# Optimization experiments

Hardware: AMD Instinct MI355X
Metric: run time of the kernel (lower is better)

The kernel has to match this reference:

```python
import jax, jax.numpy as jnp
import numpy as np

B, S, D_MODEL, N_HEADS = 4, 2048, 2048, 16
HEAD_DIM = D_MODEL // N_HEADS  # 128
ROT_HALF = HEAD_DIM // 2       # 64


def _make_rope(max_pos, half_dim, base=10000.0):
    inv_freq = 1.0 / (base ** (np.arange(0, half_dim, dtype=np.float32) / half_dim))
    t = np.arange(max_pos, dtype=np.float32)
    freqs = np.outer(t, inv_freq)  # (max_pos, half_dim)
    return jnp.asarray(np.cos(freqs)), jnp.asarray(np.sin(freqs))


def setup_inputs() -> dict:
    key = jax.random.key(0)
    k1, k2, k3 = jax.random.split(key, 3)
    x = jax.random.normal(k1, (B, S, D_MODEL), dtype=jnp.float32)
    w_qkv = jax.random.normal(k2, (D_MODEL, 3 * D_MODEL), dtype=jnp.float32) * (D_MODEL ** -0.5)
    b_qkv = jnp.zeros((3 * D_MODEL,), dtype=jnp.float32)
    w_out = jax.random.normal(k3, (D_MODEL, D_MODEL), dtype=jnp.float32) * (D_MODEL ** -0.5)
    b_out = jnp.zeros((D_MODEL,), dtype=jnp.float32)
    rotary_cos, rotary_sin = _make_rope(S, ROT_HALF)
    return {"x": x, "w_qkv": w_qkv, "b_qkv": b_qkv, "w_out": w_out,
            "b_out": b_out, "rotary_cos": rotary_cos, "rotary_sin": rotary_sin}


def _apply_rope(q, k, cos, sin):
    # q, k: (B, H, S, Dh); cos, sin: (S, Dh//2)
    cos = cos[None, None, :, :]
    sin = sin[None, None, :, :]

    def _rotate(t):
        even = t[..., 0::2]
        odd = t[..., 1::2]
        r_even = even * cos - odd * sin
        r_odd = even * sin + odd * cos
        return jnp.stack([r_even, r_odd], axis=-1).reshape(t.shape)

    return _rotate(q), _rotate(k)


def reference(x, w_qkv, b_qkv, w_out, b_out, rotary_cos, rotary_sin):
    batch, seq, _ = x.shape
    scale = HEAD_DIM ** -0.5
    # Fused QKV projection, split into heads
    qkv = x @ w_qkv + b_qkv                                   # (B, S, 3*D)
    qkv = qkv.reshape(batch, seq, 3, N_HEADS, HEAD_DIM)
    qkv = jnp.transpose(qkv, (2, 0, 3, 1, 4))                 # (3, B, H, S, Dh)
    q, k, v = qkv[0], qkv[1], qkv[2]
    # RoPE at pos_offset = 0
    q, k = _apply_rope(q, k, rotary_cos[:seq], rotary_sin[:seq])
    # Causal scaled dot-product attention
    scores = jnp.einsum("bhqd,bhkd->bhqk", q, k) * scale      # (B, H, S, S)
    causal = jnp.tril(jnp.ones((seq, seq), dtype=bool))
    scores = jnp.where(causal, scores, jnp.finfo(scores.dtype).min)
    attn = jax.nn.softmax(scores, axis=-1)
    out = jnp.einsum("bhqk,bhkd->bhqd", attn, v)              # (B, H, S, Dh)
    out = jnp.transpose(out, (0, 2, 1, 3)).reshape(batch, seq, D_MODEL)
    return out @ w_out + b_out
```

## Files before the change

kernel.cpp:

```cpp
#include <hip/hip_runtime.h>
#include <stdint.h>

#define B_  4
#define S_  2048
#define DM_ 2048
#define NH_ 16
#define HD_ 128

typedef unsigned short u16;
typedef unsigned int   u32;
typedef __attribute__((ext_vector_type(8))) short short8;
typedef __attribute__((ext_vector_type(8))) unsigned short u16x8;
typedef __attribute__((ext_vector_type(4))) float f32x4;

__device__ __forceinline__ u16 f2b(float f){
  union { float f; unsigned u; } v; v.f = f;
  return (u16)((v.u + 0x7fffu + ((v.u >> 16) & 1u)) >> 16);
}
__device__ __forceinline__ float b2f(u16 b){
  union { unsigned u; float f; } v; v.u = ((unsigned)b) << 16; return v.f;
}
__device__ __forceinline__ void gld_lds16(const void* g, void* l){
  __builtin_amdgcn_global_load_lds(
    (const __attribute__((address_space(1))) unsigned int*)(uintptr_t)g,
    (__attribute__((address_space(3))) unsigned int*)(uintptr_t)l, 16, 0, 0);
}

__global__ void k_convert(const float* __restrict__ in, u16* __restrict__ out, int n){
  int i = (blockIdx.x * 256 + threadIdx.x) * 8;
  if (i >= n) return;
  float4 a = *(const float4*)(in + i);
  float4 b = *(const float4*)(in + i + 4);
  u16x8 o;
  o[0]=f2b(a.x); o[1]=f2b(a.y); o[2]=f2b(a.z); o[3]=f2b(a.w);
  o[4]=f2b(b.x); o[5]=f2b(b.y); o[6]=f2b(b.z); o[7]=f2b(b.w);
  *(u16x8*)(out + i) = o;
}

__global__ void k_transpose_cvt(const float* __restrict__ in, u16* __restrict__ out,
                                int R, int C){
  __shared__ u16 tile[32][33];
  int tx = threadIdx.x, ty = threadIdx.y;
  int c0 = blockIdx.x * 32, r0 = blockIdx.y * 32;
  #pragma unroll
  for (int i = 0; i < 4; i++){
    int r = r0 + ty + i * 8;
    tile[ty + i*8][tx] = f2b(in[(size_t)r * C + c0 + tx]);
  }
  __syncthreads();
  #pragma unroll
  for (int i = 0; i < 4; i++){
    int c = c0 + ty + i * 8;
    out[(size_t)c * R + r0 + tx] = tile[tx][ty + i*8];
  }
}

template<int EPI>
__global__ __launch_bounds__(256, 2) void k_gemm_bt(
    const u16* __restrict__ A, const u16* __restrict__ BT,
    const float* __restrict__ bias,
    u16* __restrict__ Qd, u16* __restrict__ Kd, u16* __restrict__ Vd,
    float* __restrict__ Cout)
{
  __shared__ u16 As[128 * 32];
  __shared__ u16 Bs[128 * 32];
  const int lane = threadIdx.x & 63;
  const int wid  = threadIdx.x >> 6;
  const int wr = wid >> 1, wc = wid & 1;
  const int m0 = blockIdx.x * 128;
  const int n0 = blockIdx.y * 128;
  f32x4 acc[4][4] = {};
  const int fr = lane & 15;
  const int ks = (lane >> 4) * 8;

  for (int k0 = 0; k0 < 2048; k0 += 32){
    __syncthreads();
    #pragma unroll
    for (int t = 0; t < 2; t++){
      const int ob  = wid * 2048 + t * 1024 + lane * 16;
      const int row = ob >> 6, colb = ob & 63;
      gld_lds16(A  + (size_t)(m0 + row) * 2048 + k0 + (colb >> 1),
                (char*)As + wid * 2048 + t * 1024);
      gld_lds16(BT + (size_t)(n0 + row) * 2048 + k0 + (colb >> 1),
                (char*)Bs + wid * 2048 + t * 1024);
    }
    __syncthreads();
    short8 af[4], bf[4];
    #pragma unroll
    for (int i = 0; i < 4; i++) af[i] = *(const short8*)&As[(wr*64 + i*16 + fr)*32 + ks];
    #pragma unroll
    for (int i = 0; i < 4; i++) bf[i] = *(const short8*)&Bs[(wc*64 + i*16 + fr)*32 + ks];
    #pragma unroll
    for (int i = 0; i < 4; i++)
      #pragma unroll
      for (int j = 0; j < 4; j++)
        acc[i][j] = __builtin_amdgcn_mfma_f32_16x16x32_bf16(af[i], bf[j], acc[i][j], 0, 0, 0);
  }

  const int rowb = m0 + wr*64 + (lane >> 4) * 4;
  const int colb = n0 + wc*64 + (lane & 15);
  #pragma unroll
  for (int ni = 0; ni < 4; ni++){
    const int col = colb + ni * 16;
    const float bv = bias[col];
    if (EPI == 0){
      const int qkv = col >> 11, hd = col & 2047, h = hd >> 7, d = hd & 127;
      u16* dst = (qkv == 0) ? Qd : ((qkv == 1) ? Kd : Vd);
      #pragma unroll
      for (int mi = 0; mi < 4; mi++){
        f32x4 c = acc[mi][ni];
        #pragma unroll
        for (int j = 0; j < 4; j++){
          const int row = rowb + mi * 16 + j;
          const int b = row >> 11, s = row & 2047;
          size_t idx;
          if (qkv == 2) idx = ((size_t)((b * NH_ + h) * HD_ + d)) * S_ + s;
          else          idx = ((size_t)((b * NH_ + h) * S_  + s)) * HD_ + d;
          dst[idx] = f2b(c[j] + bv);
        }
      }
    } else {
      #pragma unroll
      for (int mi = 0; mi < 4; mi++){
        f32x4 c = acc[mi][ni];
        #pragma unroll
        for (int j = 0; j < 4; j++){
          const int row = rowb + mi * 16 + j;
          Cout[(size_t)row * 2048 + col] = c[j] + bv;
        }
      }
    }
  }
}

__global__ void k_rope(u16* __restrict__ Qb, u16* __restrict__ Kb,
                       const float* __restrict__ rc, const float* __restrict__ rs){
  const int gid = blockIdx.x * 256 + threadIdx.x;
  const int seg = gid & 3;
  const int row = gid >> 2;
  const int NR  = B_ * NH_ * S_;
  u16* base = (row < NR) ? (Qb + (size_t)row * HD_) : (Kb + (size_t)(row - NR) * HD_);
  const int s  = row & (S_ - 1);
  const int d0 = seg * 32;
  u16x8 v[4];
  #pragma unroll
  for (int t = 0; t < 4; t++) v[t] = *(u16x8*)(base + d0 + t * 8);
  float c[16], sn[16];
  const float4* cp = (const float4*)(rc + (size_t)s * 64 + seg * 16);
  const float4* sp = (const float4*)(rs + (size_t)s * 64 + seg * 16);
  #pragma unroll
  for (int t = 0; t < 4; t++){
    float4 cv = cp[t], sv = sp[t];
    c[t*4+0]=cv.x; c[t*4+1]=cv.y; c[t*4+2]=cv.z; c[t*4+3]=cv.w;
    sn[t*4+0]=sv.x; sn[t*4+1]=sv.y; sn[t*4+2]=sv.z; sn[t*4+3]=sv.w;
  }
  #pragma unroll
  for (int p = 0; p < 16; p++){
    int t = p >> 2, l = (2 * p) & 7;
    float e = b2f(v[t][l]), o = b2f(v[t][l + 1]);
    v[t][l]     = f2b(e * c[p] - o * sn[p]);
    v[t][l + 1] = f2b(e * sn[p] + o * c[p]);
  }
  #pragma unroll
  for (int t = 0; t < 4; t++) *(u16x8*)(base + d0 + t * 8) = v[t];
}

#define KVB 64
__global__ __launch_bounds__(256, 4) void k_attn(
    const u16* __restrict__ Qb, const u16* __restrict__ Kb,
    const u16* __restrict__ Vtb, u16* __restrict__ Ob)
{
  const int bh = blockIdx.y;
  const int qt = (int)gridDim.x - 1 - (int)blockIdx.x;
  const int lane = threadIdx.x & 63, wid = threadIdx.x >> 6;
  const int q = lane & 15, g = lane >> 4;
  const int b = bh >> 4, h = bh & 15;
  const u16* Qp = Qb  + (size_t)bh * S_ * HD_;
  const u16* Kp = Kb  + (size_t)bh * S_ * HD_;
  const u16* Vp = Vtb + (size_t)bh * HD_ * S_;
  __shared__ u16 Ks[KVB * HD_];
  __shared__ u16 Vs[HD_ * KVB];

  const int q0 = qt * 64 + wid * 16;
  const int q_abs = q0 + q;

  short8 qf[4];
  {
    const u16* qrow = Qp + (size_t)(q0 + q) * HD_ + g * 8;
    #pragma unroll
    for (int kk = 0; kk < 4; kk++) qf[kk] = *(const short8*)(qrow + kk * 32);
  }
  f32x4 oacc[8] = {};
  float mrun = -__builtin_inff(), lrun = 0.f;
  const float scale = 0.08838834764831845f;
  const int nt = qt + 1;
  const int base16 = wid * 256 + lane;

  for (int it = 0; it < nt; ++it){
    const int kv0 = it * KVB;
    __syncthreads();
    #pragma unroll
    for (int c = 0; c < 4; c++){
      const int idx = base16 + c * 64;
      const int r  = idx >> 4, y  = idx & 15;
      const int r2 = idx >> 3, y2 = idx & 7;
      gld_lds16(Kp + (size_t)(kv0 + r) * HD_ + ((y ^ (r & 15)) << 3),
                (char*)Ks + ((wid * 256 + c * 64) << 4));
      gld_lds16(Vp + (size_t)r2 * S_ + kv0 + ((y2 ^ (r2 & 7)) << 3),
                (char*)Vs + ((wid * 256 + c * 64) << 4));
    }
    __syncthreads();
    if (kv0 > q0 + 15) continue;

    f32x4 sacc[4] = {};
    const char* ksb = (const char*)Ks + q * 256;
    #pragma unroll
    for (int nf = 0; nf < 4; nf++)
      #pragma unroll
      for (int kk = 0; kk < 4; kk++){
        const int slot = (4 * kk + g) ^ q;
        short8 kf = *(const short8*)(ksb + nf * 4096 + slot * 16);
        sacc[nf] = __builtin_amdgcn_mfma_f32_16x16x32_bf16(kf, qf[kk], sacc[nf], 0, 0, 0);
      }

    float p[4][4];
    float pmax = -__builtin_inff();
    #pragma unroll
    for (int nf = 0; nf < 4; nf++)
      #pragma unroll
      for (int j = 0; j < 4; j++){
        const int k_abs = kv0 + nf * 16 + 4 * g + j;
        const float sv = (k_abs <= q_abs) ? sacc[nf][j] * scale : -__builtin_inff();
        p[nf][j] = sv;
        pmax = fmaxf(pmax, sv);
      }
    pmax = fmaxf(pmax, __shfl_xor(pmax, 16));
    pmax = fmaxf(pmax, __shfl_xor(pmax, 32));
    const float mnew = fmaxf(mrun, pmax);
    const float sc = __expf(mrun - mnew);
    float rsum = 0.f;
    #pragma unroll
    for (int nf = 0; nf < 4; nf++)
      #pragma unroll
      for (int j = 0; j < 4; j++){
        const float e = __expf(p[nf][j] - mnew);
        p[nf][j] = e; rsum += e;
      }
    rsum += __shfl_xor(rsum, 16);
    rsum += __shfl_xor(rsum, 32);
    lrun = lrun * sc + rsum; mrun = mnew;

    float scr[4];
    #pragma unroll
    for (int j = 0; j < 4; j++) scr[j] = __shfl(sc, 4 * g + j);
    #pragma unroll
    for (int m = 0; m < 8; m++)
      #pragma unroll
      for (int j = 0; j < 4; j++) oacc[m][j] *= scr[j];

    u32 pk[4][2];
    #pragma unroll
    for (int nf = 0; nf < 4; nf++)
      #pragma unroll
      for (int t = 0; t < 2; t++)
        pk[nf][t] = (u32)f2b(p[nf][2*t]) | ((u32)f2b(p[nf][2*t+1]) << 16);

    const int s0 = q + (((2 * g    ) & 3) << 4);
    const int s1 = q + (((2 * g + 1) & 3) << 4);
    const bool hi = (g >> 1) != 0;
    #pragma unroll
    for (int c = 0; c < 2; c++){
      const int A0 = __shfl((int)pk[2*c][0], s0), B0 = __shfl((int)pk[2*c+1][0], s0);
      const int A1 = __shfl((int)pk[2*c][1], s0), B1 = __shfl((int)pk[2*c+1][1], s0);
      const int A2 = __shfl((int)pk[2*c][0], s1), B2 = __shfl((int)pk[2*c+1][0], s1);
      const int A3 = __shfl((int)pk[2*c][1], s1), B3 = __shfl((int)pk[2*c+1][1], s1);
      union { int w[4]; short8 v; } pa;
      pa.w[0] = hi ? B0 : A0;
      pa.w[1] = hi ? B1 : A1;
      pa.w[2] = hi ? B2 : A2;
      pa.w[3] = hi ? B3 : A3;
      const int slot = (4 * c + g) ^ (q & 7);
      const char* vsb = (const char*)Vs + q * 128 + slot * 16;
      #pragma unroll
      for (int m = 0; m < 8; m++){
        short8 vf = *(const short8*)(vsb + m * 2048);
        oacc[m] = __builtin_amdgcn_mfma_f32_16x16x32_bf16(pa.v, vf, oacc[m], 0, 0, 0);
      }
    }
  }

  const float inv = 1.0f / lrun;
  #pragma unroll
  for (int j = 0; j < 4; j++){
    const float linv = __shfl(inv, 4 * g + j);
    const int row = q0 + 4 * g + j;
    u16* orow = Ob + ((size_t)(b * S_ + row) * DM_) + h * HD_ + q;
    #pragma unroll
    for (int m = 0; m < 8; m++)
      orow[m * 16] = f2b(oacc[m][j] * linv);
  }
}

extern "C" void kernel_launch(void* const* d_in, const int* in_sizes, int n_in,
                              void* d_out, int out_size, void* d_ws, size_t ws_size,
                              hipStream_t stream) {
  const float* x     = (const float*)d_in[0];
  const float* w_qkv = (const float*)d_in[1];
  const float* b_qkv = (const float*)d_in[2];
  const float* w_out = (const float*)d_in[3];
  const float* b_out = (const float*)d_in[4];
  const float* rc    = (const float*)d_in[5];
  const float* rs    = (const float*)d_in[6];
  char* ws = (char*)d_ws;
  u16* xb    = (u16*)(ws);
  u16* wqkvT = (u16*)(ws + 33554432ull);
  u16* woutT = (u16*)(ws + 58720256ull);
  u16* Qb    = (u16*)(ws + 67108864ull);
  u16* Kb    = (u16*)(ws + 100663296ull);
  u16* Vt    = (u16*)(ws + 134217728ull);
  u16* AO    = xb;
  float* out = (float*)d_out;

  k_convert<<<8192, 256, 0, stream>>>(x, xb, 16777216);
  k_transpose_cvt<<<dim3(192, 64), dim3(32, 8), 0, stream>>>(w_qkv, wqkvT, 2048, 6144);
  k_transpose_cvt<<<dim3(64, 64),  dim3(32, 8), 0, stream>>>(w_out, woutT, 2048, 2048);
  k_gemm_bt<0><<<dim3(64, 48), 256, 0, stream>>>(xb, wqkvT, b_qkv, Qb, Kb, Vt, nullptr);
  k_rope<<<4096, 256, 0, stream>>>(Qb, Kb, rc, rs);
  k_attn<<<dim3(32, 64), 256, 0, stream>>>(Qb, Kb, Vt, AO);
  k_gemm_bt<1><<<dim3(64, 16), 256, 0, stream>>>(AO, woutT, b_out, nullptr, nullptr, nullptr, out);
}
```

Measured before the change: 801.6 us.

## Switch attention to 32x32x16 MFMA with 128-query blocks per workgroup

Rewrites the flash-attention kernel so each wave handles 32 query rows using 32x32x16 bf16 MFMA instead of 16x16x32. Each workgroup now covers 128 queries, which halves the grid and doubles reuse of each K/V tile loaded into LDS. Softmax reductions need fewer cross-lane shuffles. The cost is higher register pressure (launch bounds drop to 2 blocks per SIMD group) and a coarser causal tail, so more work is wasted on masked tiles near the diagonal.

```diff
diff --git a/kernel.cpp b/kernel.cpp
--- a/kernel.cpp
+++ b/kernel.cpp
@@ -12,6 +12,7 @@
 typedef __attribute__((ext_vector_type(8))) short short8;
 typedef __attribute__((ext_vector_type(8))) unsigned short u16x8;
 typedef __attribute__((ext_vector_type(4))) float f32x4;
+typedef __attribute__((ext_vector_type(16))) float f32x16;
 
 __device__ __forceinline__ u16 f2b(float f){
   union { float f; unsigned u; } v; v.f = f;
@@ -166,14 +167,14 @@
 }
 
 #define KVB 64
-__global__ __launch_bounds__(256, 4) void k_attn(
+__global__ __launch_bounds__(256, 2) void k_attn(
     const u16* __restrict__ Qb, const u16* __restrict__ Kb,
     const u16* __restrict__ Vtb, u16* __restrict__ Ob)
 {
   const int bh = blockIdx.y;
   const int qt = (int)gridDim.x - 1 - (int)blockIdx.x;
   const int lane = threadIdx.x & 63, wid = threadIdx.x >> 6;
-  const int q = lane & 15, g = lane >> 4;
+  const int q = lane & 31, hi = lane >> 5;
   const int b = bh >> 4, h = bh & 15;
   const u16* Qp = Qb  + (size_t)bh * S_ * HD_;
   const u16* Kp = Kb  + (size_t)bh * S_ * HD_;
@@ -181,19 +182,19 @@
   __shared__ u16 Ks[KVB * HD_];
   __shared__ u16 Vs[HD_ * KVB];
 
-  const int q0 = qt * 64 + wid * 16;
-  const int q_abs = q0 + q;
-
-  short8 qf[4];
+  const int q0w  = qt * 128 + wid * 32;
+  const int q_abs = q0w + q;
+
+  short8 qf[8];
   {
-    const u16* qrow = Qp + (size_t)(q0 + q) * HD_ + g * 8;
-    #pragma unroll
-    for (int kk = 0; kk < 4; kk++) qf[kk] = *(const short8*)(qrow + kk * 32);
-  }
-  f32x4 oacc[8] = {};
+    const u16* qrow = Qp + (size_t)q_abs * HD_ + hi * 8;
+    #pragma unroll
+    for (int s = 0; s < 8; s++) qf[s] = *(const short8*)(qrow + s * 16);
+  }
+  f32x16 oacc[4] = {};
   float mrun = -__builtin_inff(), lrun = 0.f;
   const float scale = 0.08838834764831845f;
-  const int nt = qt + 1;
+  const int nt = 2 * qt + 2;
   const int base16 = wid * 256 + lane;
 
   for (int it = 0; it < nt; ++it){
@@ -210,94 +211,91 @@
                 (char*)Vs + ((wid * 256 + c * 64) << 4));
     }
     __syncthreads();
-    if (kv0 > q0 + 15) continue;
-
-    f32x4 sacc[4] = {};
-    const char* ksb = (const char*)Ks + q * 256;
-    #pragma unroll
-    for (int nf = 0; nf < 4; nf++)
-      #pragma unroll
-      for (int kk = 0; kk < 4; kk++){
-        const int slot = (4 * kk + g) ^ q;
-        short8 kf = *(const short8*)(ksb + nf * 4096 + slot * 16);
-        sacc[nf] = __builtin_amdgcn_mfma_f32_16x16x32_bf16(kf, qf[kk], sacc[nf], 0, 0, 0);
-      }
-
-    float p[4][4];
+    if (kv0 > q0w + 31) continue;
+
+    f32x16 sacc[2] = {};
+    #pragma unroll
+    for (int s = 0; s < 8; s++)
+      #pragma unroll
+      for (int kb = 0; kb < 2; kb++){
+        const int row  = kb * 32 + q;
+        const int slot = (2 * s + hi) ^ (q & 15);
+        short8 kf = *(const short8*)((const char*)Ks + row * 256 + slot * 16);
+        sacc[kb] = __builtin_amdgcn_mfma_f32_32x32x16_bf16(kf, qf[s], sacc[kb], 0, 0, 0);
+      }
+
     float pmax = -__builtin_inff();
     #pragma unroll
-    for (int nf = 0; nf < 4; nf++)
-      #pragma unroll
-      for (int j = 0; j < 4; j++){
-        const int k_abs = kv0 + nf * 16 + 4 * g + j;
-        const float sv = (k_abs <= q_abs) ? sacc[nf][j] * scale : -__builtin_inff();
-        p[nf][j] = sv;
+    for (int kb = 0; kb < 2; kb++)
+      #pragma unroll
+      for (int i = 0; i < 16; i++){
+        const int k_abs = kv0 + kb * 32 + (i & 3) + 8 * (i >> 2) + 4 * hi;
+        const float sv = (k_abs <= q_abs) ? sacc[kb][i] * scale : -__builtin_inff();
+        sacc[kb][i] = sv;
         pmax = fmaxf(pmax, sv);
       }
-    pmax = fmaxf(pmax, __shfl_xor(pmax, 16));
     pmax = fmaxf(pmax, __shfl_xor(pmax, 32));
     const float mnew = fmaxf(mrun, pmax);
     const float sc = __expf(mrun - mnew);
     float rsum = 0.f;
     #pragma unroll
-    for (int nf = 0; nf < 4; nf++)
-      #pragma unroll
-      for (int j = 0; j < 4; j++){
-        const float e = __expf(p[nf][j] - mnew);
-        p[nf][j] = e; rsum += e;
-      }
-    rsum += __shfl_xor(rsum, 16);
+    for (int kb = 0; kb < 2; kb++)
+      #pragma unroll
+      for (int i = 0; i < 16; i++){
+        const float e = __expf(sacc[kb][i] - mnew);
+        sacc[kb][i] = e; rsum += e;
+      }
     rsum += __shfl_xor(rsum, 32);
     lrun = lrun * sc + rsum; mrun = mnew;
 
-    float scr[4];
-    #pragma unroll
-    for (int j = 0; j < 4; j++) scr[j] = __shfl(sc, 4 * g + j);
-    #pragma unroll
-    for (int m = 0; m < 8; m++)
-      #pragma unroll
-      for (int j = 0; j < 4; j++) oacc[m][j] *= scr[j];
-
-    u32 pk[4][2];
-    #pragma unroll
-    for (int nf = 0; nf < 4; nf++)
-      #pragma unroll
-      for (int t = 0; t < 2; t++)
-        pk[nf][t] = (u32)f2b(p[nf][2*t]) | ((u32)f2b(p[nf][2*t+1]) << 16);
-
-    const int s0 = q + (((2 * g    ) & 3) << 4);
-    const int s1 = q + (((2 * g + 1) & 3) << 4);
-    const bool hi = (g >> 1) != 0;
-    #pragma unroll
-    for (int c = 0; c < 2; c++){
-      const int A0 = __shfl((int)pk[2*c][0], s0), B0 = __shfl((int)pk[2*c+1][0], s0);
-      const int A1 = __shfl((int)pk[2*c][1], s0), B1 = __shfl((int)pk[2*c+1][1], s0);
-      const int A2 = __shfl((int)pk[2*c][0], s1), B2 = __shfl((int)pk[2*c+1][0], s1);
-      const int A3 = __shfl((int)pk[2*c][1], s1), B3 = __shfl((int)pk[2*c+1][1], s1);
+    #pragma unroll
+    for (int i = 0; i < 16; i++){
+      const float s_i = __shfl(sc, (i & 3) + 8 * (i >> 2) + 4 * hi);
+      #pragma unroll
+      for (int n4 = 0; n4 < 4; n4++) oacc[n4][i] *= s_i;
+    }
+
+    u32 wds[2][8];
+    #pragma unroll
+    for (int kb = 0; kb < 2; kb++)
+      #pragma unroll
+      for (int t = 0; t < 8; t++)
+        wds[kb][t] = (u32)f2b(sacc[kb][2*t]) | ((u32)f2b(sacc[kb][2*t+1]) << 16);
+
+    #pragma unroll
+    for (int sp = 0; sp < 4; sp++){
+      const int kb = sp >> 1, hh = sp & 1;
+      const u32 w0 = wds[kb][4*hh+0], w1 = wds[kb][4*hh+1];
+      const u32 w2 = wds[kb][4*hh+2], w3 = wds[kb][4*hh+3];
+      const int x0 = __shfl((int)w0, q + 32);
+      const int x1 = __shfl((int)w1, q + 32);
+      const int y0 = __shfl((int)w2, q);
+      const int y1 = __shfl((int)w3, q);
       union { int w[4]; short8 v; } pa;
-      pa.w[0] = hi ? B0 : A0;
-      pa.w[1] = hi ? B1 : A1;
-      pa.w[2] = hi ? B2 : A2;
-      pa.w[3] = hi ? B3 : A3;
-      const int slot = (4 * c + g) ^ (q & 7);
-      const char* vsb = (const char*)Vs + q * 128 + slot * 16;
-      #pragma unroll
-      for (int m = 0; m < 8; m++){
-        short8 vf = *(const short8*)(vsb + m * 2048);
-        oacc[m] = __builtin_amdgcn_mfma_f32_16x16x32_bf16(pa.v, vf, oacc[m], 0, 0, 0);
+      pa.w[0] = hi ? y0 : (int)w0;
+      pa.w[1] = hi ? y1 : (int)w1;
+      pa.w[2] = hi ? (int)w2 : x0;
+      pa.w[3] = hi ? (int)w3 : x1;
+      #pragma unroll
+      for (int n4 = 0; n4 < 4; n4++){
+        const int d = n4 * 32 + q;
+        const int slot = (2 * sp + hi) ^ (d & 7);
+        short8 vf = *(const short8*)((const char*)Vs + d * 128 + slot * 16);
+        oacc[n4] = __builtin_amdgcn_mfma_f32_32x32x16_bf16(pa.v, vf, oacc[n4], 0, 0, 0);
       }
     }
   }
 
   const float inv = 1.0f / lrun;
   #pragma unroll
-  for (int j = 0; j < 4; j++){
-    const float linv = __shfl(inv, 4 * g + j);
-    const int row = q0 + 4 * g + j;
+  for (int i = 0; i < 16; i++){
+    const int r = (i & 3) + 8 * (i >> 2) + 4 * hi;
+    const float linv = __shfl(inv, r);
+    const int row = q0w + r;
     u16* orow = Ob + ((size_t)(b * S_ + row) * DM_) + h * HD_ + q;
     #pragma unroll
-    for (int m = 0; m < 8; m++)
-      orow[m * 16] = f2b(oacc[m][j] * linv);
+    for (int n4 = 0; n4 < 4; n4++)
+      orow[n4 * 32] = f2b(oacc[n4][i] * linv);
   }
 }
 
@@ -326,6 +324,6 @@
   k_transpose_cvt<<<dim3(64, 64),  dim3(32, 8), 0, stream>>>(w_out, woutT, 2048, 2048);
   k_gemm_bt<0><<<dim3(64, 48), 256, 0, stream>>>(xb, wqkvT, b_qkv, Qb, Kb, Vt, nullptr);
   k_rope<<<4096, 256, 0, stream>>>(Qb, Kb, rc, rs);
-  k_attn<<<dim3(32, 64), 256, 0, stream>>>(Qb, Kb, Vt, AO);
+  k_attn<<<dim3(16, 64), 256, 0, stream>>>(Qb, Kb, Vt, AO);
   k_gemm_bt<1><<<dim3(64, 16), 256, 0, stream>>>(AO, woutT, b_out, nullptr, nullptr, nullptr, out);
 }
```

Result: faster. 747.2 us (-6.8%).
